# Kernel tuning notes

Measured on AMD Instinct MI355X. Metric: run time of the kernel, lower is better.

## Reference

```python
import jax, jax.numpy as jnp
import numpy as np

TOKENS, IN_F, OUT_F = 16, 4096, 11008


def setup_inputs() -> dict:
    key = jax.random.key(0)
    k1, k2, k3, k4 = jax.random.split(key, 4)
    x = jax.random.normal(k1, (TOKENS, IN_F), dtype=jnp.float32)
    weight_int8 = jax.random.randint(k2, (OUT_F, IN_F), 0, 127, dtype=jnp.int32)
    # per-row scale, clamped >= 1e-8 as in the torch module
    scale = jnp.maximum(jax.random.uniform(k3, (OUT_F, 1), dtype=jnp.float32) * 0.02, 1e-8)
    bias = jax.random.normal(k4, (OUT_F,), dtype=jnp.float32)
    return {"x": x, "weight_int8": weight_int8, "scale": scale, "bias": bias}


def reference(x, weight_int8, scale, bias):
    # dequantize: [out, in] fp32 weight, cast to activation dtype
    w = (weight_int8.astype(jnp.float32) * scale).astype(x.dtype)
    # F.linear: x @ w.T + bias
    return jnp.einsum('ti,oi->to', x, w) + bias.astype(x.dtype)
```

## Files before the change

kernel.cpp:

```cpp
#include <hip/hip_runtime.h>
#include <hip/hip_bf16.h>

typedef float f32x4 __attribute__((ext_vector_type(4)));
typedef short short8 __attribute__((ext_vector_type(8)));

constexpr int TOKENS = 16;
constexpr int IN_F   = 4096;
constexpr int OUT_F  = 11008;
constexpr int WAVES  = 4;
constexpr int SEG_K  = IN_F / WAVES;
constexpr int NTILES = OUT_F / 16;

__device__ __forceinline__ short bf16_rne(float f) {
    unsigned u = __builtin_bit_cast(unsigned, f);
    u += 0x7fffu + ((u >> 16) & 1u);
    return (short)(u >> 16);
}
__device__ __forceinline__ short bf16_from_int(int v) {
    float f = (float)v;
    return (short)(__builtin_bit_cast(unsigned, f) >> 16);
}

__global__ __launch_bounds__(256) void Int8Linear_kernel(
    const float* __restrict__ x,
    const int*   __restrict__ w,
    const float* __restrict__ scale,
    const float* __restrict__ bias,
    float*       __restrict__ out)
{
    const int tid  = threadIdx.x;
    const int wave = tid >> 6;
    const int lane = tid & 63;
    const int m    = lane & 15;
    const int g    = lane >> 4;
    const int n0   = blockIdx.x * 16;

    const float* xp = x + (size_t)m * IN_F + wave * SEG_K + g * 8;
    const int*   wp = w + (size_t)(n0 + m) * IN_F + wave * SEG_K + g * 8;

    f32x4 acc = {0.f, 0.f, 0.f, 0.f};

    #pragma unroll 4
    for (int kb = 0; kb < SEG_K / 32; ++kb) {
        float4 xa = *(const float4*)xp;
        float4 xb = *(const float4*)(xp + 4);
        int4   wa = *(const int4*)wp;
        int4   wb = *(const int4*)(wp + 4);
        xp += 32; wp += 32;

        short8 a, b;
        a[0] = bf16_rne(xa.x); a[1] = bf16_rne(xa.y);
        a[2] = bf16_rne(xa.z); a[3] = bf16_rne(xa.w);
        a[4] = bf16_rne(xb.x); a[5] = bf16_rne(xb.y);
        a[6] = bf16_rne(xb.z); a[7] = bf16_rne(xb.w);

        b[0] = bf16_from_int(wa.x); b[1] = bf16_from_int(wa.y);
        b[2] = bf16_from_int(wa.z); b[3] = bf16_from_int(wa.w);
        b[4] = bf16_from_int(wb.x); b[5] = bf16_from_int(wb.y);
        b[6] = bf16_from_int(wb.z); b[7] = bf16_from_int(wb.w);

        acc = __builtin_amdgcn_mfma_f32_16x16x32_bf16(a, b, acc, 0, 0, 0);
    }

    __shared__ float red[WAVES][16][16];
    #pragma unroll
    for (int r = 0; r < 4; ++r)
        red[wave][g * 4 + r][m] = acc[r];
    __syncthreads();

    const int row = tid >> 4;
    const int col = tid & 15;
    float s = red[0][row][col] + red[1][row][col]
            + red[2][row][col] + red[3][row][col];
    const int o = n0 + col;
    out[(size_t)row * OUT_F + o] = s * scale[o] + bias[o];
}

extern "C" void kernel_launch(void* const* d_in, const int* in_sizes, int n_in,
                              void* d_out, int out_size, void* d_ws, size_t ws_size,
                              hipStream_t stream) {
    const float* x     = (const float*)d_in[0];
    const int*   w     = (const int*)d_in[1];
    const float* scale = (const float*)d_in[2];
    const float* bias  = (const float*)d_in[3];
    float*       out   = (float*)d_out;

    Int8Linear_kernel<<<NTILES, 256, 0, stream>>>(x, w, scale, bias, out);
}
```

Baseline: 48.52 us.

## Pre-convert activations to bf16 and use single-wave blocks without reduction

Adds a separate kernel that converts x to bf16 once into workspace, so the main kernel loads packed bf16 activations instead of converting floats on every pass. The main kernel now uses one wave per 16-column tile, walking the full K dimension. This drops the shared-memory cross-wave reduction and the barrier, and the epilogue writes straight from the accumulators. In exchange there are 4x fewer waves and an extra launch, which may reduce memory-level parallelism on the weight stream.

```diff
diff --git a/kernel.cpp b/kernel.cpp
--- a/kernel.cpp
+++ b/kernel.cpp
@@ -7,53 +7,54 @@
 constexpr int TOKENS = 16;
 constexpr int IN_F   = 4096;
 constexpr int OUT_F  = 11008;
-constexpr int WAVES  = 4;
-constexpr int SEG_K  = IN_F / WAVES;
 constexpr int NTILES = OUT_F / 16;
 
-__device__ __forceinline__ short bf16_rne(float f) {
+__device__ __forceinline__ unsigned short bf16_rne(float f) {
     unsigned u = __builtin_bit_cast(unsigned, f);
     u += 0x7fffu + ((u >> 16) & 1u);
-    return (short)(u >> 16);
+    return (unsigned short)(u >> 16);
 }
 __device__ __forceinline__ short bf16_from_int(int v) {
     float f = (float)v;
     return (short)(__builtin_bit_cast(unsigned, f) >> 16);
 }
 
-__global__ __launch_bounds__(256) void Int8Linear_kernel(
-    const float* __restrict__ x,
+__global__ __launch_bounds__(256) void cvt_x_kernel(
+    const float* __restrict__ x, unsigned short* __restrict__ xb)
+{
+    const int i = (blockIdx.x * 256 + threadIdx.x) * 4;
+    float4 v = *(const float4*)(x + i);
+    ushort4 o;
+    o.x = bf16_rne(v.x); o.y = bf16_rne(v.y);
+    o.z = bf16_rne(v.z); o.w = bf16_rne(v.w);
+    *(ushort4*)(xb + i) = o;
+}
+
+__global__ __launch_bounds__(64) void Int8Linear_kernel(
+    const unsigned short* __restrict__ xb,
     const int*   __restrict__ w,
     const float* __restrict__ scale,
     const float* __restrict__ bias,
     float*       __restrict__ out)
 {
-    const int tid  = threadIdx.x;
-    const int wave = tid >> 6;
-    const int lane = tid & 63;
+    const int lane = threadIdx.x;
     const int m    = lane & 15;
     const int g    = lane >> 4;
     const int n0   = blockIdx.x * 16;
 
-    const float* xp = x + (size_t)m * IN_F + wave * SEG_K + g * 8;
-    const int*   wp = w + (size_t)(n0 + m) * IN_F + wave * SEG_K + g * 8;
+    const unsigned short* xp = xb + (size_t)m * IN_F + g * 8;
+    const int*            wp = w  + (size_t)(n0 + m) * IN_F + g * 8;
 
     f32x4 acc = {0.f, 0.f, 0.f, 0.f};
 
-    #pragma unroll 4
-    for (int kb = 0; kb < SEG_K / 32; ++kb) {
-        float4 xa = *(const float4*)xp;
-        float4 xb = *(const float4*)(xp + 4);
+    #pragma unroll 8
+    for (int kb = 0; kb < IN_F / 32; ++kb) {
+        short8 a = *(const short8*)xp;
         int4   wa = *(const int4*)wp;
         int4   wb = *(const int4*)(wp + 4);
         xp += 32; wp += 32;
 
-        short8 a, b;
-        a[0] = bf16_rne(xa.x); a[1] = bf16_rne(xa.y);
-        a[2] = bf16_rne(xa.z); a[3] = bf16_rne(xa.w);
-        a[4] = bf16_rne(xb.x); a[5] = bf16_rne(xb.y);
-        a[6] = bf16_rne(xb.z); a[7] = bf16_rne(xb.w);
-
+        short8 b;
         b[0] = bf16_from_int(wa.x); b[1] = bf16_from_int(wa.y);
         b[2] = bf16_from_int(wa.z); b[3] = bf16_from_int(wa.w);
         b[4] = bf16_from_int(wb.x); b[5] = bf16_from_int(wb.y);
@@ -62,18 +63,14 @@
         acc = __builtin_amdgcn_mfma_f32_16x16x32_bf16(a, b, acc, 0, 0, 0);
     }
 
-    __shared__ float red[WAVES][16][16];
+    const int o = n0 + m;
+    const float sc = scale[o];
+    const float bi = bias[o];
     #pragma unroll
-    for (int r = 0; r < 4; ++r)
-        red[wave][g * 4 + r][m] = acc[r];
-    __syncthreads();
-
-    const int row = tid >> 4;
-    const int col = tid & 15;
-    float s = red[0][row][col] + red[1][row][col]
-            + red[2][row][col] + red[3][row][col];
-    const int o = n0 + col;
-    out[(size_t)row * OUT_F + o] = s * scale[o] + bias[o];
+    for (int r = 0; r < 4; ++r) {
+        const int row = g * 4 + r;
+        out[(size_t)row * OUT_F + o] = acc[r] * sc + bi;
+    }
 }
 
 extern "C" void kernel_launch(void* const* d_in, const int* in_sizes, int n_in,
@@ -84,6 +81,8 @@
     const float* scale = (const float*)d_in[2];
     const float* bias  = (const float*)d_in[3];
     float*       out   = (float*)d_out;
+    unsigned short* xb = (unsigned short*)d_ws;
 
-    Int8Linear_kernel<<<NTILES, 256, 0, stream>>>(x, w, scale, bias, out);
+    cvt_x_kernel<<<64, 256, 0, stream>>>(x, xb);
+    Int8Linear_kernel<<<NTILES, 64, 0, stream>>>(xb, w, scale, bias, out);
 }
```

Result: slower. 58.66 us (+20.9%).
